# Kernel optimization log

Measured on AMD Instinct MI355X. Metric: run time of the kernel, lower is better.

Reference implementation:

```python
import itertools
import jax, jax.numpy as jnp
import numpy as np

B, N_TOK, DIM = 256, 196, 384
H, KD, D, RES = 8, 32, 128, 14
HID = (2 * KD + D) * H  # 1536


def _build_bias_idxs():
    # Faithful reproduction of the LeViT relative-offset index table.
    points = list(itertools.product(range(RES), range(RES)))
    offsets = {}
    idxs = []
    for p1 in points:
        for p2 in points:
            off = (abs(p1[0] - p2[0]), abs(p1[1] - p2[1]))
            if off not in offsets:
                offsets[off] = len(offsets)
            idxs.append(offsets[off])
    return np.asarray(idxs, dtype=np.int64).reshape(len(points), len(points)), len(offsets)


def setup_inputs() -> dict:
    key = jax.random.key(0)
    k0, k1, k2, k3, k4, k5 = jax.random.split(key, 6)
    idxs_np, n_off = _build_bias_idxs()  # n_off == 196 for RES=14
    return {
        "x": jax.random.normal(k0, (B, N_TOK, DIM), dtype=jnp.float32),
        "Wqkv": jax.random.normal(k1, (HID, DIM), dtype=jnp.float32) * 0.02,
        "bqkv": jax.random.normal(k2, (HID,), dtype=jnp.float32) * 0.02,
        "Wproj": jax.random.normal(k3, (DIM, H * D), dtype=jnp.float32) * 0.02,
        "bproj": jax.random.normal(k4, (DIM,), dtype=jnp.float32) * 0.02,
        "ab_table": jax.random.normal(k5, (H, n_off), dtype=jnp.float32) * 0.02,
        "bias_idxs": jnp.asarray(idxs_np),  # [N, N] int64
    }


def reference(x, Wqkv, bqkv, Wproj, bproj, ab_table, bias_idxs):
    Bsz, N, _ = x.shape
    scale = KD ** -0.5
    qkv = x @ Wqkv.T + bqkv                      # [B, N, HID]
    qkv = qkv.reshape(Bsz, N, H, 2 * KD + D)
    q = qkv[..., :KD]                             # [B, N, H, KD]
    k = qkv[..., KD:2 * KD]                       # [B, N, H, KD]
    v = qkv[..., 2 * KD:]                         # [B, N, H, D]
    bias = ab_table[:, bias_idxs]                 # [H, N, N] gather
    attn = jnp.einsum("bnhk,bmhk->bhnm", q, k) * scale + bias
    attn = jax.nn.softmax(attn, axis=-1)
    out = jnp.einsum("bhnm,bmhd->bnhd", attn, v).reshape(Bsz, N, H * D)
    return out @ Wproj.T + bproj                  # [B, N, DIM]
```

## Files before the change

kernel.cpp:

```cpp
#include <hip/hip_runtime.h>
#include <math.h>

#define B_SZ 256
#define N_TOKENS 196
#define DIM 384
#define NH 8
#define QKV_ST 1536
#define HID 1536
#define CTX_ST 1024
#define VT_ST 208

typedef short s16x8_base __attribute__((ext_vector_type(8)));
typedef s16x8_base __attribute__((may_alias)) s16x8;
typedef float f32x4_base __attribute__((ext_vector_type(4)));
typedef f32x4_base __attribute__((may_alias)) f32x4;

__device__ inline unsigned short f2b(float f) {
  union { float f; unsigned int u; } v; v.f = f;
  unsigned int r = (v.u + 0x7FFFu + ((v.u >> 16) & 1u)) >> 16;
  return (unsigned short)r;
}

__global__ __launch_bounds__(256)
void cvt_f32_bf16(const float* __restrict__ in, unsigned short* __restrict__ out, int n4) {
  int i = blockIdx.x * 256 + threadIdx.x;
  const int stride = gridDim.x * 256;
  for (; i < n4; i += stride) {
    float4 v = ((const float4*)in)[i];
    ushort4 o;
    o.x = f2b(v.x); o.y = f2b(v.y); o.z = f2b(v.z); o.w = f2b(v.w);
    ((ushort4*)out)[i] = o;
  }
}

__global__ __launch_bounds__(256)
void zero_vt_pad(unsigned short* __restrict__ vt, int total) {
  int i = blockIdx.x * 256 + threadIdx.x;
  if (i < total) {
    const int c = i % 12, rr = i / 12;
    vt[(size_t)rr * VT_ST + 196 + c] = 0;
  }
}

template <int MODE>
__global__ __launch_bounds__(256)
void gemm_bf16_bt(const unsigned short* __restrict__ A,
                  const unsigned short* __restrict__ Bm,
                  const float* __restrict__ bias,
                  void* __restrict__ C, unsigned short* __restrict__ vt,
                  int M, int N, int K) {
  __shared__ unsigned short As[128][32];
  __shared__ unsigned short Bs[128][32];
  const int tid = threadIdx.x;
  const int lane = tid & 63, wave = tid >> 6;
  const int quad = lane >> 4, l15 = lane & 15;
  const int ntile = N >> 7;
  const int bx = blockIdx.x % ntile, by = blockIdx.x / ntile;
  const int row0 = by << 7, col0 = bx << 7;

  const int srow = tid >> 1, soff = (tid & 1) << 4;
  const unsigned short* Ag = A + (size_t)(row0 + srow) * K + soff;
  const unsigned short* Bg = Bm + (size_t)(col0 + srow) * K + soff;

  const int wr = (wave >> 1) << 6, wc = (wave & 1) << 6;

  f32x4 zero = {0.f, 0.f, 0.f, 0.f};
  f32x4 acc[4][4];
#pragma unroll
  for (int i = 0; i < 4; ++i)
#pragma unroll
    for (int j = 0; j < 4; ++j) acc[i][j] = zero;

  s16x8 a0 = *(const s16x8*)(Ag + 0);
  s16x8 a1 = *(const s16x8*)(Ag + 8);
  s16x8 b0 = *(const s16x8*)(Bg + 0);
  s16x8 b1 = *(const s16x8*)(Bg + 8);

  for (int k0 = 0; k0 < K; k0 += 32) {
    __syncthreads();
    *(s16x8*)&As[srow][soff] = a0;
    *(s16x8*)&As[srow][soff + 8] = a1;
    *(s16x8*)&Bs[srow][soff] = b0;
    *(s16x8*)&Bs[srow][soff + 8] = b1;
    __syncthreads();
    if (k0 + 32 < K) {
      a0 = *(const s16x8*)(Ag + k0 + 32);
      a1 = *(const s16x8*)(Ag + k0 + 40);
      b0 = *(const s16x8*)(Bg + k0 + 32);
      b1 = *(const s16x8*)(Bg + k0 + 40);
    }
    s16x8 af[4], bf[4];
#pragma unroll
    for (int i = 0; i < 4; ++i) {
      af[i] = *(const s16x8*)&As[wr + i * 16 + l15][quad * 8];
      bf[i] = *(const s16x8*)&Bs[wc + i * 16 + l15][quad * 8];
    }
#pragma unroll
    for (int i = 0; i < 4; ++i)
#pragma unroll
      for (int j = 0; j < 4; ++j)
        acc[i][j] = __builtin_amdgcn_mfma_f32_16x16x32_bf16(bf[j], af[i], acc[i][j], 0, 0, 0);
  }

#pragma unroll
  for (int j = 0; j < 4; ++j) {
    const int colb = col0 + wc + j * 16 + quad * 4;
    const f32x4 bj = *(const f32x4*)&bias[colb];
    if (MODE == 0) {
#pragma unroll
      for (int i = 0; i < 4; ++i) {
        const int row = row0 + wr + i * 16 + l15;
        f32x4 v = acc[i][j] + bj;
        *(f32x4*)((float*)C + (size_t)row * N + colb) = v;
      }
    } else {
      const int hh = colb / 192;
      const int c192 = colb - hh * 192;
      if (c192 < 64) {
#pragma unroll
        for (int i = 0; i < 4; ++i) {
          const int row = row0 + wr + i * 16 + l15;
          f32x4 v = acc[i][j] + bj;
          ushort4 o;
          o.x = f2b(v[0]); o.y = f2b(v[1]); o.z = f2b(v[2]); o.w = f2b(v[3]);
          *(ushort4*)((unsigned short*)C + (size_t)row * N + colb) = o;
        }
      } else {
        const int d = c192 - 64;
#pragma unroll
        for (int i = 0; i < 4; ++i) {
          const int row = row0 + wr + i * 16 + l15;
          const int bl = row / 196;
          const int n = row - bl * 196;
          f32x4 v = acc[i][j] + bj;
          unsigned short* vp = vt + ((size_t)((bl * 8 + hh) * 128 + d)) * VT_ST + n;
#pragma unroll
          for (int r = 0; r < 4; ++r) vp[(size_t)r * VT_ST] = f2b(v[r]);
        }
      }
    }
  }
}

__global__ __launch_bounds__(256)
void attn_mfma(const unsigned short* __restrict__ qkv,
               const unsigned short* __restrict__ vt,
               const float* __restrict__ ab,
               unsigned short* __restrict__ ctx) {
  __shared__ unsigned short Pm[112][232];
  __shared__ float inv_s[112];
  __shared__ float ab_s[196];

  const int bh = blockIdx.x;
  const int b = bh >> 3, h = bh & 7;
  const int tid = threadIdx.x;
  const int lane = tid & 63, w = tid >> 6;
  const int quad = lane >> 4, l15 = lane & 15;
  const float scale = 0.17677669529663687f;

  const unsigned short* qbase = qkv + (size_t)b * N_TOKENS * QKV_ST + h * 192;
  const int pr = (l15 & 3) + ((l15 >> 2) << 3);
  const unsigned short* vgw = vt + ((size_t)bh * 128 + w * 32 + pr) * VT_ST + quad * 8;
  unsigned short* ctxp = ctx + (size_t)b * N_TOKENS * CTX_ST + h * 128;

  if (tid < 196) ab_s[tid] = ab[h * 196 + tid];
  if (tid < 112) {
#pragma unroll
    for (int c = 208; c < 232; ++c) Pm[tid][c] = 0;
  }

  f32x4 zero = {0.f, 0.f, 0.f, 0.f};

  for (int chunk = 0; chunk < 2; ++chunk) {
    const int nbase = chunk * 112;
    __syncthreads();

    const int ntr = (w < 3) ? 2 : 1;
    for (int t2 = 0; t2 < ntr; ++t2) {
      const int rowt = w * 32 + t2 * 16;
      s16x8 aq = *(const s16x8*)(qbase + (size_t)(nbase + rowt + l15) * QKV_ST + quad * 8);
      f32x4 sacc[13];
#pragma unroll
      for (int j = 0; j < 13; ++j) {
        s16x8 bk = *(const s16x8*)(qbase + (size_t)(j * 16 + l15) * QKV_ST + 32 + quad * 8);
        sacc[j] = __builtin_amdgcn_mfma_f32_16x16x32_bf16(aq, bk, zero, 0, 0, 0);
      }
      int rn4[4], cn4[4];
#pragma unroll
      for (int r = 0; r < 4; ++r) {
        const int n = nbase + rowt + quad * 4 + r;
        const int nn = n < 196 ? n : 195;
        rn4[r] = nn / 14;
        cn4[r] = nn - rn4[r] * 14;
      }
      float mx[4] = {-1e30f, -1e30f, -1e30f, -1e30f};
#pragma unroll
      for (int j = 0; j < 13; ++j) {
        const int m = j * 16 + l15;
        const int mc = m < 196 ? m : 195;
        const int rm = mc / 14, cm = mc - rm * 14;
#pragma unroll
        for (int r = 0; r < 4; ++r) {
          int dr = rn4[r] - rm; dr = dr < 0 ? -dr : dr;
          int dc = cn4[r] - cm; dc = dc < 0 ? -dc : dc;
          float s = fmaf(sacc[j][r], scale, ab_s[dr * 14 + dc]);
          s = (m < 196) ? s : -1e30f;
          sacc[j][r] = s;
          mx[r] = fmaxf(mx[r], s);
        }
      }
#pragma unroll
      for (int o = 8; o > 0; o >>= 1)
#pragma unroll
        for (int r = 0; r < 4; ++r) mx[r] = fmaxf(mx[r], __shfl_xor(mx[r], o));
      float sm[4] = {0.f, 0.f, 0.f, 0.f};
#pragma unroll
      for (int j = 0; j < 13; ++j)
#pragma unroll
        for (int r = 0; r < 4; ++r) {
          float e = __expf(sacc[j][r] - mx[r]);
          sm[r] += e;
          Pm[rowt + quad * 4 + r][j * 16 + l15] = f2b(e);
        }
#pragma unroll
      for (int o = 8; o > 0; o >>= 1)
#pragma unroll
        for (int r = 0; r < 4; ++r) sm[r] += __shfl_xor(sm[r], o);
      if (l15 == 0) {
#pragma unroll
        for (int r = 0; r < 4; ++r) inv_s[rowt + quad * 4 + r] = 1.f / sm[r];
      }
    }
    __syncthreads();

    f32x4 a0[7], a1[7];
#pragma unroll
    for (int i = 0; i < 7; ++i) { a0[i] = zero; a1[i] = zero; }
    s16x8 va0 = *(const s16x8*)(vgw + 0);
    s16x8 va1 = *(const s16x8*)(vgw + 4 * VT_ST);
#pragma unroll
    for (int ks = 0; ks < 7; ++ks) {
      s16x8 nva0, nva1;
      if (ks < 6) {
        nva0 = *(const s16x8*)(vgw + (ks + 1) * 32);
        nva1 = *(const s16x8*)(vgw + 4 * VT_ST + (ks + 1) * 32);
      }
#pragma unroll
      for (int i = 0; i < 7; ++i) {
        s16x8 pb = *(const s16x8*)&Pm[i * 16 + l15][ks * 32 + quad * 8];
        a0[i] = __builtin_amdgcn_mfma_f32_16x16x32_bf16(va0, pb, a0[i], 0, 0, 0);
        a1[i] = __builtin_amdgcn_mfma_f32_16x16x32_bf16(va1, pb, a1[i], 0, 0, 0);
      }
      va0 = nva0; va1 = nva1;
    }

#pragma unroll
    for (int i = 0; i < 7; ++i) {
      const int n = nbase + i * 16 + l15;
      if (n < 196) {
        const float is = inv_s[i * 16 + l15];
        s16x8 o;
        o[0] = (short)f2b(a0[i][0] * is); o[1] = (short)f2b(a0[i][1] * is);
        o[2] = (short)f2b(a0[i][2] * is); o[3] = (short)f2b(a0[i][3] * is);
        o[4] = (short)f2b(a1[i][0] * is); o[5] = (short)f2b(a1[i][1] * is);
        o[6] = (short)f2b(a1[i][2] * is); o[7] = (short)f2b(a1[i][3] * is);
        *(s16x8*)(ctxp + (size_t)n * CTX_ST + w * 32 + quad * 8) = o;
      }
    }
  }
}

extern "C" void kernel_launch(void* const* d_in, const int* in_sizes, int n_in,
                              void* d_out, int out_size, void* d_ws, size_t ws_size,
                              hipStream_t stream) {
  const float* x     = (const float*)d_in[0];
  const float* Wqkv  = (const float*)d_in[1];
  const float* bqkv  = (const float*)d_in[2];
  const float* Wproj = (const float*)d_in[3];
  const float* bproj = (const float*)d_in[4];
  const float* ab    = (const float*)d_in[5];
  float* out = (float*)d_out;

  const size_t szWq = 589824, szWp = 393216, szX = (size_t)B_SZ * N_TOKENS * DIM;
  const size_t fixedB = (szWq + szWp + szX) * 2;
  const size_t perB = (212992ULL + 301056ULL + 200704ULL) * 2;
  int Bs = 256;
  while (Bs > 32 && fixedB + (size_t)Bs * perB > ws_size) Bs >>= 1;

  unsigned short* Wqb  = (unsigned short*)d_ws;
  unsigned short* Wpb  = Wqb + szWq;
  unsigned short* xb   = Wpb + szWp;
  unsigned short* vtb  = xb + szX;
  unsigned short* qkvb = vtb + (size_t)Bs * 212992;
  unsigned short* ctxb = qkvb + (size_t)Bs * 301056;

  cvt_f32_bf16<<<dim3(576), dim3(256), 0, stream>>>(Wqkv, Wqb, (int)(szWq / 4));
  cvt_f32_bf16<<<dim3(384), dim3(256), 0, stream>>>(Wproj, Wpb, (int)(szWp / 4));
  cvt_f32_bf16<<<dim3(4096), dim3(256), 0, stream>>>(x, xb, (int)(szX / 4));
  {
    const int total = Bs * 8 * 128 * 12;
    zero_vt_pad<<<dim3((total + 255) / 256), dim3(256), 0, stream>>>(vtb, total);
  }

  const int nslice = B_SZ / Bs;
  const int Ms = Bs * N_TOKENS;
  for (int s = 0; s < nslice; ++s) {
    const unsigned short* xs = xb + (size_t)s * Ms * DIM;
    float* outs = out + (size_t)s * Ms * DIM;
    gemm_bf16_bt<1><<<dim3((Ms / 128) * (HID / 128)), dim3(256), 0, stream>>>(
        xs, Wqb, bqkv, qkvb, vtb, Ms, HID, DIM);
    attn_mfma<<<dim3(Bs * 8), dim3(256), 0, stream>>>(qkvb, vtb, ab, ctxb);
    gemm_bf16_bt<0><<<dim3((Ms / 128) * (DIM / 128)), dim3(256), 0, stream>>>(
        ctxb, Wpb, bproj, outs, nullptr, Ms, DIM, CTX_ST);
  }
}
```

Before: 526.1 us.

## Split attention per (batch, head) into four 64-row query chunks across blocks

The attention kernel used to process both 112-row query chunks in a loop inside one block per (batch, head). It now launches four blocks per (batch, head), each handling 64 query rows (the last handles 16), with smaller shared memory and a launch-bounds hint of 4 blocks per CU. The aim is more parallelism and occupancy. In exchange, the K and V loads and the bias-table setup are repeated in each block. A QKV padding region is added to the workspace because the last chunk reads query rows past 196.

```diff
diff --git a/kernel.cpp b/kernel.cpp
--- a/kernel.cpp
+++ b/kernel.cpp
@@ -142,21 +142,124 @@
   }
 }
 
-__global__ __launch_bounds__(256)
+template <int NT>
+__device__ __forceinline__ void attn_chunk64(
+    const int nbase, const unsigned short* __restrict__ qbase,
+    const unsigned short* __restrict__ vgw,
+    const float* __restrict__ ab_s, unsigned short* __restrict__ ctxp,
+    unsigned short (*__restrict__ Pm)[232], float* __restrict__ inv_s,
+    const int w, const int quad, const int l15) {
+  const float scale = 0.17677669529663687f;
+  f32x4 zero = {0.f, 0.f, 0.f, 0.f};
+
+  if (w < NT) {
+    const int rowt = w * 16;
+    s16x8 aq = *(const s16x8*)(qbase + (size_t)(nbase + rowt + l15) * QKV_ST + quad * 8);
+    f32x4 sacc[13];
+#pragma unroll
+    for (int j = 0; j < 13; ++j) {
+      s16x8 bk = *(const s16x8*)(qbase + (size_t)(j * 16 + l15) * QKV_ST + 32 + quad * 8);
+      sacc[j] = __builtin_amdgcn_mfma_f32_16x16x32_bf16(aq, bk, zero, 0, 0, 0);
+    }
+    int rn4[4], cn4[4];
+#pragma unroll
+    for (int r = 0; r < 4; ++r) {
+      const int n = nbase + rowt + quad * 4 + r;
+      const int nn = n < 196 ? n : 195;
+      rn4[r] = nn / 14;
+      cn4[r] = nn - rn4[r] * 14;
+    }
+    float mx[4] = {-1e30f, -1e30f, -1e30f, -1e30f};
+#pragma unroll
+    for (int j = 0; j < 13; ++j) {
+      const int m = j * 16 + l15;
+      const int mc = m < 196 ? m : 195;
+      const int rm = mc / 14, cm = mc - rm * 14;
+#pragma unroll
+      for (int r = 0; r < 4; ++r) {
+        int dr = rn4[r] - rm; dr = dr < 0 ? -dr : dr;
+        int dc = cn4[r] - cm; dc = dc < 0 ? -dc : dc;
+        float s = fmaf(sacc[j][r], scale, ab_s[dr * 14 + dc]);
+        s = (m < 196) ? s : -1e30f;
+        sacc[j][r] = s;
+        mx[r] = fmaxf(mx[r], s);
+      }
+    }
+#pragma unroll
+    for (int o = 8; o > 0; o >>= 1)
+#pragma unroll
+      for (int r = 0; r < 4; ++r) mx[r] = fmaxf(mx[r], __shfl_xor(mx[r], o));
+    float sm[4] = {0.f, 0.f, 0.f, 0.f};
+#pragma unroll
+    for (int j = 0; j < 13; ++j)
+#pragma unroll
+      for (int r = 0; r < 4; ++r) {
+        float e = __expf(sacc[j][r] - mx[r]);
+        sm[r] += e;
+        Pm[rowt + quad * 4 + r][j * 16 + l15] = f2b(e);
+      }
+#pragma unroll
+    for (int o = 8; o > 0; o >>= 1)
+#pragma unroll
+      for (int r = 0; r < 4; ++r) sm[r] += __shfl_xor(sm[r], o);
+    if (l15 == 0) {
+#pragma unroll
+      for (int r = 0; r < 4; ++r) inv_s[rowt + quad * 4 + r] = 1.f / sm[r];
+    }
+  }
+  __syncthreads();
+
+  f32x4 a0[NT], a1[NT];
+#pragma unroll
+  for (int i = 0; i < NT; ++i) { a0[i] = zero; a1[i] = zero; }
+  s16x8 va0 = *(const s16x8*)(vgw + 0);
+  s16x8 va1 = *(const s16x8*)(vgw + 4 * VT_ST);
+#pragma unroll
+  for (int ks = 0; ks < 7; ++ks) {
+    s16x8 nva0, nva1;
+    if (ks < 6) {
+      nva0 = *(const s16x8*)(vgw + (ks + 1) * 32);
+      nva1 = *(const s16x8*)(vgw + 4 * VT_ST + (ks + 1) * 32);
+    }
+#pragma unroll
+    for (int i = 0; i < NT; ++i) {
+      s16x8 pb = *(const s16x8*)&Pm[i * 16 + l15][ks * 32 + quad * 8];
+      a0[i] = __builtin_amdgcn_mfma_f32_16x16x32_bf16(va0, pb, a0[i], 0, 0, 0);
+      a1[i] = __builtin_amdgcn_mfma_f32_16x16x32_bf16(va1, pb, a1[i], 0, 0, 0);
+    }
+    va0 = nva0; va1 = nva1;
+  }
+
+#pragma unroll
+  for (int i = 0; i < NT; ++i) {
+    const int n = nbase + i * 16 + l15;
+    if (n < 196) {
+      const float is = inv_s[i * 16 + l15];
+      s16x8 o;
+      o[0] = (short)f2b(a0[i][0] * is); o[1] = (short)f2b(a0[i][1] * is);
+      o[2] = (short)f2b(a0[i][2] * is); o[3] = (short)f2b(a0[i][3] * is);
+      o[4] = (short)f2b(a1[i][0] * is); o[5] = (short)f2b(a1[i][1] * is);
+      o[6] = (short)f2b(a1[i][2] * is); o[7] = (short)f2b(a1[i][3] * is);
+      *(s16x8*)(ctxp + (size_t)n * CTX_ST + w * 32 + quad * 8) = o;
+    }
+  }
+}
+
+__global__ __launch_bounds__(256, 4)
 void attn_mfma(const unsigned short* __restrict__ qkv,
                const unsigned short* __restrict__ vt,
                const float* __restrict__ ab,
                unsigned short* __restrict__ ctx) {
-  __shared__ unsigned short Pm[112][232];
-  __shared__ float inv_s[112];
+  __shared__ unsigned short Pm[64][232];
+  __shared__ float inv_s[64];
   __shared__ float ab_s[196];
 
-  const int bh = blockIdx.x;
+  const int bhc = blockIdx.x;
+  const int bh = bhc >> 2, chunk = bhc & 3;
   const int b = bh >> 3, h = bh & 7;
   const int tid = threadIdx.x;
   const int lane = tid & 63, w = tid >> 6;
   const int quad = lane >> 4, l15 = lane & 15;
-  const float scale = 0.17677669529663687f;
 
   const unsigned short* qbase = qkv + (size_t)b * N_TOKENS * QKV_ST + h * 192;
   const int pr = (l15 & 3) + ((l15 >> 2) << 3);
@@ -164,110 +267,16 @@
   unsigned short* ctxp = ctx + (size_t)b * N_TOKENS * CTX_ST + h * 128;
 
   if (tid < 196) ab_s[tid] = ab[h * 196 + tid];
-  if (tid < 112) {
+  if (tid < 64) {
 #pragma unroll
     for (int c = 208; c < 232; ++c) Pm[tid][c] = 0;
   }
-
-  f32x4 zero = {0.f, 0.f, 0.f, 0.f};
-
-  for (int chunk = 0; chunk < 2; ++chunk) {
-    const int nbase = chunk * 112;
-    __syncthreads();
-
-    const int ntr = (w < 3) ? 2 : 1;
-    for (int t2 = 0; t2 < ntr; ++t2) {
-      const int rowt = w * 32 + t2 * 16;
-      s16x8 aq = *(const s16x8*)(qbase + (size_t)(nbase + rowt + l15) * QKV_ST + quad * 8);
-      f32x4 sacc[13];
-#pragma unroll
-      for (int j = 0; j < 13; ++j) {
-        s16x8 bk = *(const s16x8*)(qbase + (size_t)(j * 16 + l15) * QKV_ST + 32 + quad * 8);
-        sacc[j] = __builtin_amdgcn_mfma_f32_16x16x32_bf16(aq, bk, zero, 0, 0, 0);
-      }
-      int rn4[4], cn4[4];
-#pragma unroll
-      for (int r = 0; r < 4; ++r) {
-        const int n = nbase + rowt + quad * 4 + r;
-        const int nn = n < 196 ? n : 195;
-        rn4[r] = nn / 14;
-        cn4[r] = nn - rn4[r] * 14;
-      }
-      float mx[4] = {-1e30f, -1e30f, -1e30f, -1e30f};
-#pragma unroll
-      for (int j = 0; j < 13; ++j) {
-        const int m = j * 16 + l15;
-        const int mc = m < 196 ? m : 195;
-        const int rm = mc / 14, cm = mc - rm * 14;
-#pragma unroll
-        for (int r = 0; r < 4; ++r) {
-          int dr = rn4[r] - rm; dr = dr < 0 ? -dr : dr;
-          int dc = cn4[r] - cm; dc = dc < 0 ? -dc : dc;
-          float s = fmaf(sacc[j][r], scale, ab_s[dr * 14 + dc]);
-          s = (m < 196) ? s : -1e30f;
-          sacc[j][r] = s;
-          mx[r] = fmaxf(mx[r], s);
-        }
-      }
-#pragma unroll
-      for (int o = 8; o > 0; o >>= 1)
-#pragma unroll
-        for (int r = 0; r < 4; ++r) mx[r] = fmaxf(mx[r], __shfl_xor(mx[r], o));
-      float sm[4] = {0.f, 0.f, 0.f, 0.f};
-#pragma unroll
-      for (int j = 0; j < 13; ++j)
-#pragma unroll
-        for (int r = 0; r < 4; ++r) {
-          float e = __expf(sacc[j][r] - mx[r]);
-          sm[r] += e;
-          Pm[rowt + quad * 4 + r][j * 16 + l15] = f2b(e);
-        }
-#pragma unroll
-      for (int o = 8; o > 0; o >>= 1)
-#pragma unroll
-        for (int r = 0; r < 4; ++r) sm[r] += __shfl_xor(sm[r], o);
-      if (l15 == 0) {
-#pragma unroll
-        for (int r = 0; r < 4; ++r) inv_s[rowt + quad * 4 + r] = 1.f / sm[r];
-      }
-    }
-    __syncthreads();
-
-    f32x4 a0[7], a1[7];
-#pragma unroll
-    for (int i = 0; i < 7; ++i) { a0[i] = zero; a1[i] = zero; }
-    s16x8 va0 = *(const s16x8*)(vgw + 0);
-    s16x8 va1 = *(const s16x8*)(vgw + 4 * VT_ST);
-#pragma unroll
-    for (int ks = 0; ks < 7; ++ks) {
-      s16x8 nva0, nva1;
-      if (ks < 6) {
-        nva0 = *(const s16x8*)(vgw + (ks + 1) * 32);
-        nva1 = *(const s16x8*)(vgw + 4 * VT_ST + (ks + 1) * 32);
-      }
-#pragma unroll
-      for (int i = 0; i < 7; ++i) {
-        s16x8 pb = *(const s16x8*)&Pm[i * 16 + l15][ks * 32 + quad * 8];
-        a0[i] = __builtin_amdgcn_mfma_f32_16x16x32_bf16(va0, pb, a0[i], 0, 0, 0);
-        a1[i] = __builtin_amdgcn_mfma_f32_16x16x32_bf16(va1, pb, a1[i], 0, 0, 0);
-      }
-      va0 = nva0; va1 = nva1;
-    }
-
-#pragma unroll
-    for (int i = 0; i < 7; ++i) {
-      const int n = nbase + i * 16 + l15;
-      if (n < 196) {
-        const float is = inv_s[i * 16 + l15];
-        s16x8 o;
-        o[0] = (short)f2b(a0[i][0] * is); o[1] = (short)f2b(a0[i][1] * is);
-        o[2] = (short)f2b(a0[i][2] * is); o[3] = (short)f2b(a0[i][3] * is);
-        o[4] = (short)f2b(a1[i][0] * is); o[5] = (short)f2b(a1[i][1] * is);
-        o[6] = (short)f2b(a1[i][2] * is); o[7] = (short)f2b(a1[i][3] * is);
-        *(s16x8*)(ctxp + (size_t)n * CTX_ST + w * 32 + quad * 8) = o;
-      }
-    }
-  }
+  __syncthreads();
+
+  if (chunk < 3)
+    attn_chunk64<4>(chunk * 64, qbase, vgw, ab_s, ctxp, Pm, inv_s, w, quad, l15);
+  else
+    attn_chunk64<1>(192, qbase, vgw, ab_s, ctxp, Pm, inv_s, w, quad, l15);
 }
 
 extern "C" void kernel_launch(void* const* d_in, const int* in_sizes, int n_in,
@@ -282,7 +291,8 @@
   float* out = (float*)d_out;
 
   const size_t szWq = 589824, szWp = 393216, szX = (size_t)B_SZ * N_TOKENS * DIM;
-  const size_t fixedB = (szWq + szWp + szX) * 2;
+  const size_t QPAD = 12 * QKV_ST;
+  const size_t fixedB = (szWq + szWp + szX + QPAD) * 2;
   const size_t perB = (212992ULL + 301056ULL + 200704ULL) * 2;
   int Bs = 256;
   while (Bs > 32 && fixedB + (size_t)Bs * perB > ws_size) Bs >>= 1;
@@ -292,7 +302,7 @@
   unsigned short* xb   = Wpb + szWp;
   unsigned short* vtb  = xb + szX;
   unsigned short* qkvb = vtb + (size_t)Bs * 212992;
-  unsigned short* ctxb = qkvb + (size_t)Bs * 301056;
+  unsigned short* ctxb = qkvb + (size_t)Bs * 301056 + QPAD;
 
   cvt_f32_bf16<<<dim3(576), dim3(256), 0, stream>>>(Wqkv, Wqb, (int)(szWq / 4));
   cvt_f32_bf16<<<dim3(384), dim3(256), 0, stream>>>(Wproj, Wpb, (int)(szWp / 4));
@@ -309,7 +319,7 @@
     float* outs = out + (size_t)s * Ms * DIM;
     gemm_bf16_bt<1><<<dim3((Ms / 128) * (HID / 128)), dim3(256), 0, stream>>>(
         xs, Wqb, bqkv, qkvb, vtb, Ms, HID, DIM);
-    attn_mfma<<<dim3(Bs * 8), dim3(256), 0, stream>>>(qkvb, vtb, ab, ctxb);
+    attn_mfma<<<dim3(Bs * 8 * 4), dim3(256), 0, stream>>>(qkvb, vtb, ab, ctxb);
     gemm_bf16_bt<0><<<dim3((Ms / 128) * (DIM / 128)), dim3(256), 0, stream>>>(
         ctxb, Wpb, bproj, outs, nullptr, Ms, DIM, CTX_ST);
   }
```

New measurement: 495.5 us. -5.8%, faster.
